# Performance work log

Hardware: AMD Instinct MI355X
Metric: run time of the kernel (lower is better)

The kernel has to match this reference:

```python
import jax, jax.numpy as jnp
import numpy as np

B, T, IN_DIM = 64, 256, 256
HID, OUT_DIM = 512, 256
N_LAYERS, N_EXPERTS, N_SHARED = 2, 16, 1


def setup_inputs() -> dict:
    key = jax.random.key(0)
    ks = jax.random.split(key, 10)
    s = 0.02
    x = jax.random.normal(ks[0], (B, T, IN_DIM), dtype=jnp.float32)
    route_id = jax.random.randint(ks[1], (B,), 0, N_EXPERTS)
    Wi = jax.random.normal(ks[2], (HID, IN_DIM), dtype=jnp.float32) * s
    bi = jnp.zeros((HID,), dtype=jnp.float32)
    Wr = jax.random.normal(ks[3], (N_LAYERS, N_EXPERTS, HID, HID), dtype=jnp.float32) * s
    br = jax.random.normal(ks[4], (N_LAYERS, N_EXPERTS, HID), dtype=jnp.float32) * s
    Ws = jax.random.normal(ks[5], (N_LAYERS, N_SHARED, HID, HID), dtype=jnp.float32) * s
    bs = jax.random.normal(ks[6], (N_LAYERS, N_SHARED, HID), dtype=jnp.float32) * s
    Wo = jax.random.normal(ks[7], (OUT_DIM, HID), dtype=jnp.float32) * s
    bo = jnp.zeros((OUT_DIM,), dtype=jnp.float32)
    return {"x": x, "route_id": route_id, "Wi": Wi, "bi": bi, "Wr": Wr,
            "br": br, "Ws": Ws, "bs": bs, "Wo": Wo, "bo": bo}


def reference(x, route_id, Wi, bi, Wr, br, Ws, bs, Wo, bo):
    # flatten tokens: [B, T, in_dim] -> [N, in_dim]
    flat = x.reshape(-1, x.shape[-1])
    n_tok = flat.shape[0]
    # expand route_id: one expert id per batch element -> per token
    route = jnp.repeat(route_id, n_tok // route_id.shape[0])  # [N]
    # projector_i: Linear + ReLU (in_dim != hidden_dim path)
    h = jax.nn.relu(flat @ Wi.T + bi)  # [N, HID]
    n_layers, n_experts = Wr.shape[0], Wr.shape[1]
    for l in range(n_layers):
        # shared experts: mean of per-expert Linear outputs
        shared = (jnp.einsum('nd,shd->snh', h, Ws[l]) + bs[l][:, None, :]).mean(axis=0)
        # routed experts: top_k=1 clustering route -> each token goes to
        # exactly route[token] with weight 1.0 (grouped GEMM, loop over
        # fixed small expert set, masked combine)
        routed = jnp.zeros_like(h)
        for e in range(n_experts):
            ye = h @ Wr[l, e].T + br[l, e]  # [N, HID]
            routed = routed + jnp.where((route == e)[:, None], ye, 0.0)
        h = jax.nn.relu(shared + routed + h)
    out = h @ Wo.T + bo  # [N, OUT_DIM]
    return out.reshape(*x.shape[:-1], out.shape[-1])
```

## Files before the change

### kernel.cpp

```cpp
#include <hip/hip_runtime.h>
#include <hip/hip_bf16.h>
#include <stdint.h>


typedef __attribute__((ext_vector_type(8))) short bf16x8;
typedef __attribute__((ext_vector_type(4))) float f32x4;

#define HPAD 520
#define VMWAIT(N) asm volatile("s_waitcnt vmcnt(" #N ")" ::: "memory")

static __device__ __forceinline__ uint16_t f2bf(float f) {
  union { float f; uint32_t u; } c; c.f = f;
  uint32_t r = (c.u + 0x7FFFu + ((c.u >> 16) & 1u)) >> 16;
  return (uint16_t)r;
}
static __device__ __forceinline__ float bf2f(uint16_t h) {
  union { uint32_t u; float f; } c; c.u = ((uint32_t)h) << 16;
  return c.f;
}

static __device__ __forceinline__ void glds16(const uint16_t* g, uint16_t* l) {
  __builtin_amdgcn_global_load_lds(
      (const __attribute__((address_space(1))) uint32_t*)g,
      (__attribute__((address_space(3))) uint32_t*)l, 16, 0, 0);
}

__global__ __launch_bounds__(256) void k_prep(
    const float* __restrict__ Ws, const float* __restrict__ Wr,
    const float* __restrict__ Wi, const float* __restrict__ Wo,
    const float* __restrict__ bs, const float* __restrict__ br,
    uint16_t* __restrict__ Wcb, uint16_t* __restrict__ Wib,
    uint16_t* __restrict__ Wob, float* __restrict__ bc) {
  int bid = blockIdx.x, tid = threadIdx.x;
  if (bid < 8192) {
    int i = bid * 256 + tid;
    int idx = i * 4;
    int l = idx >> 22;
    int within = idx & (262144 - 1);
    float4 a = *(const float4*)(Ws + l * 262144 + within);
    float4 b = *(const float4*)(Wr + idx);
    ushort4 o;
    o.x = f2bf(a.x + b.x); o.y = f2bf(a.y + b.y);
    o.z = f2bf(a.z + b.z); o.w = f2bf(a.w + b.w);
    ((ushort4*)Wcb)[i] = o;
  } else if (bid < 8320) {
    int i = (bid - 8192) * 256 + tid;
    float4 v = ((const float4*)Wi)[i];
    ushort4 o;
    o.x = f2bf(v.x); o.y = f2bf(v.y); o.z = f2bf(v.z); o.w = f2bf(v.w);
    ((ushort4*)Wib)[i] = o;
  } else if (bid < 8448) {
    int i = (bid - 8320) * 256 + tid;
    float4 v = ((const float4*)Wo)[i];
    ushort4 o;
    o.x = f2bf(v.x); o.y = f2bf(v.y); o.z = f2bf(v.z); o.w = f2bf(v.w);
    ((ushort4*)Wob)[i] = o;
  } else {
    int i = (bid - 8448) * 256 + tid;
    int l = i >> 13, j = i & 511;
    bc[i] = bs[l * 512 + j] + br[i];
  }
}

template <int NT, int KK, int RESID, int F32OUT>
static __device__ __forceinline__ void gemm_phase(
    const uint16_t* __restrict__ W, const float* __restrict__ bias,
    uint16_t* h, float* __restrict__ gout, uint16_t* lS) {
  constexpr int NSTEP = KK / 32;
  constexpr int NC = NT / 8;
  constexpr int NFRAG = NC / 16;
  constexpr int LPS = NFRAG;

  const int tid = threadIdx.x;
  const int lane = tid & 63, wave = tid >> 6;
  const int lr = lane & 15, c0 = lane >> 4;
  const int rb = c0 * 4;

  uint16_t* lw = lS + wave * 4096;

  const int srow = lane >> 2;
  const int sch = (lane & 3) ^ ((lane >> 3) & 3);
  const uint16_t* wbase = W + (size_t)(wave * NC + srow) * KK + sch * 8;

  auto stage = [&](int buf, int t) {
    #pragma unroll
    for (int j = 0; j < LPS; j++)
      glds16(wbase + (size_t)j * 16 * KK + t * 32,
             lw + buf * (NC * 32) + j * 512);
  };

  stage(0, 0);
  stage(1, 1);

  f32x4 acc[4][NFRAG];
  #pragma unroll
  for (int n = 0; n < NFRAG; n++) {
    const int col = wave * NC + n * 16 + lr;
    const float bv = bias[col];
    #pragma unroll
    for (int m = 0; m < 4; m++)
      #pragma unroll
      for (int r = 0; r < 4; r++) {
        float v = bv;
        if constexpr (RESID)
          v += bf2f(h[(size_t)(m * 16 + rb + r) * HPAD + col]);
        acc[m][n][r] = v;
      }
  }

  const int bch = c0 ^ ((lr >> 1) & 3);
  const uint16_t* pB0 = lw + lr * 32 + bch * 8;
  const uint16_t* pA0 = h + (size_t)lr * HPAD + c0 * 8;

  bf16x8 a[2][4], b[2][NFRAG];

  auto frag_read = [&](int slot, int t) {
    const uint16_t* pB = pB0 + (t & 1) * (NC * 32);
    #pragma unroll
    for (int m = 0; m < 4; m++)
      a[slot][m] = *(const bf16x8*)(pA0 + (size_t)m * 16 * HPAD + t * 32);
    #pragma unroll
    for (int n = 0; n < NFRAG; n++)
      b[slot][n] = *(const bf16x8*)(pB + n * 512);
  };

  if constexpr (LPS == 4) { VMWAIT(4); } else { VMWAIT(2); }
  frag_read(0, 0);

  #pragma unroll
  for (int t = 0; t < NSTEP; t++) {
    const int cur = t & 1, nxt = cur ^ 1;
    if (t + 2 < NSTEP) stage(cur, t + 2);
    if (t + 1 < NSTEP) {
      if (t + 2 < NSTEP) {
        if constexpr (LPS == 4) { VMWAIT(4); } else { VMWAIT(2); }
      } else {
        VMWAIT(0);
      }
      frag_read(nxt, t + 1);
    }
    __builtin_amdgcn_s_setprio(1);
    #pragma unroll
    for (int m = 0; m < 4; m++)
      #pragma unroll
      for (int n = 0; n < NFRAG; n++)
        acc[m][n] = __builtin_amdgcn_mfma_f32_16x16x32_bf16(
            a[cur][m], b[cur][n], acc[m][n], 0, 0, 0);
    __builtin_amdgcn_s_setprio(0);
  }

  if constexpr (F32OUT) {
    #pragma unroll
    for (int n = 0; n < NFRAG; n++) {
      const int col = wave * NC + n * 16 + lr;
      #pragma unroll
      for (int m = 0; m < 4; m++)
        #pragma unroll
        for (int r = 0; r < 4; r++)
          gout[(size_t)(m * 16 + rb + r) * 256 + col] = acc[m][n][r];
    }
  } else {
    __syncthreads();
    #pragma unroll
    for (int n = 0; n < NFRAG; n++) {
      const int col = wave * NC + n * 16 + lr;
      #pragma unroll
      for (int m = 0; m < 4; m++)
        #pragma unroll
        for (int r = 0; r < 4; r++)
          h[(size_t)(m * 16 + rb + r) * HPAD + col] =
              f2bf(fmaxf(acc[m][n][r], 0.0f));
    }
    __syncthreads();
  }
}

__global__ __launch_bounds__(512) void k_fused(
    const float* __restrict__ x, const int* __restrict__ route,
    const uint16_t* __restrict__ Wib, const float* __restrict__ bi,
    const uint16_t* __restrict__ Wcb, const float* __restrict__ bcb,
    const uint16_t* __restrict__ Wob, const float* __restrict__ bo,
    float* __restrict__ out) {
  __shared__ uint16_t h[64 * HPAD];
  __shared__ uint16_t lS[8 * 4096];

  const int tid = threadIdx.x;
  const int bid = blockIdx.x;
  const int r = bid & 7, q = bid >> 3;
  const int batch = (q >> 2) * 8 + r;
  const int bx = batch * 4 + (q & 3);
  const int e = route[batch];

  const float* gx = x + (size_t)bx * 16384;
  #pragma unroll
  for (int j = 0; j < 8; j++) {
    int fi = j * 2048 + tid * 4;
    float4 v = *(const float4*)(gx + fi);
    int row = fi >> 8, c = fi & 255;
    ushort4 o;
    o.x = f2bf(v.x); o.y = f2bf(v.y); o.z = f2bf(v.z); o.w = f2bf(v.w);
    *(ushort4*)(h + (size_t)row * HPAD + c) = o;
  }
  __syncthreads();

  gemm_phase<512, 256, 0, 0>(Wib, bi, h, nullptr, lS);
  gemm_phase<512, 512, 1, 0>(Wcb + (size_t)e * 262144, bcb + e * 512,
                             h, nullptr, lS);
  gemm_phase<512, 512, 1, 0>(Wcb + (size_t)(16 + e) * 262144,
                             bcb + (16 + e) * 512, h, nullptr, lS);
  gemm_phase<256, 512, 0, 1>(Wob, bo, h, out + (size_t)bx * 16384, lS);
}

extern "C" void kernel_launch(void* const* d_in, const int* in_sizes, int n_in,
                              void* d_out, int out_size, void* d_ws, size_t ws_size,
                              hipStream_t stream) {
  const float* x     = (const float*)d_in[0];
  const int*   route = (const int*)d_in[1];
  const float* Wi    = (const float*)d_in[2];
  const float* bi    = (const float*)d_in[3];
  const float* Wr    = (const float*)d_in[4];
  const float* br    = (const float*)d_in[5];
  const float* Ws    = (const float*)d_in[6];
  const float* bs    = (const float*)d_in[7];
  const float* Wo    = (const float*)d_in[8];
  const float* bo    = (const float*)d_in[9];

  char* ws = (char*)d_ws;
  uint16_t* Wib = (uint16_t*)(ws);
  uint16_t* Wcb = (uint16_t*)(ws + 262144);
  uint16_t* Wob = (uint16_t*)(ws + 17039360);
  float*    bc  = (float*)   (ws + 17301504);

  k_prep<<<8512, 256, 0, stream>>>(Ws, Wr, Wi, Wo, bs, br,
                                   Wcb, Wib, Wob, bc);
  k_fused<<<256, 512, 0, stream>>>(x, route, Wib, bi, Wcb, bc, Wob, bo,
                                   (float*)d_out);
}
```

Before: 50.40 us.

## Triple-buffer weight staging and XOR-swizzle the activation tile in LDS

Weight staging goes from double to triple buffering: three K-steps are prefetched into LDS, with adjusted vmcnt waits and an lgkmcnt wait before each buffer is reused. The padded activation tile (HPAD 520) becomes an unpadded 512-wide layout with an XOR chunk swizzle, and the input conversion now writes 16-byte swizzled chunks. The aim is to hide more global-load latency and avoid LDS bank conflicts without padding. In exchange, LDS use per block grows, and the extra lgkmcnt(0) waits may stall the pipeline.

```diff
diff --git a/kernel.cpp b/kernel.cpp
--- a/kernel.cpp
+++ b/kernel.cpp
@@ -6,8 +6,8 @@
 typedef __attribute__((ext_vector_type(8))) short bf16x8;
 typedef __attribute__((ext_vector_type(4))) float f32x4;
 
-#define HPAD 520
 #define VMWAIT(N) asm volatile("s_waitcnt vmcnt(" #N ")" ::: "memory")
+#define LGKM0() asm volatile("s_waitcnt lgkmcnt(0)" ::: "memory")
 
 static __device__ __forceinline__ uint16_t f2bf(float f) {
   union { float f; uint32_t u; } c; c.f = f;
@@ -23,6 +23,10 @@
   __builtin_amdgcn_global_load_lds(
       (const __attribute__((address_space(1))) uint32_t*)g,
       (__attribute__((address_space(3))) uint32_t*)l, 16, 0, 0);
+}
+
+static __device__ __forceinline__ int hidx(int row, int col) {
+  return row * 512 + ((((col >> 3) ^ (row & 7)) << 3) | (col & 7));
 }
 
 __global__ __launch_bounds__(256) void k_prep(
@@ -75,8 +79,9 @@
   const int lane = tid & 63, wave = tid >> 6;
   const int lr = lane & 15, c0 = lane >> 4;
   const int rb = c0 * 4;
-
-  uint16_t* lw = lS + wave * 4096;
+  const int hsw = lr & 7;
+
+  uint16_t* lw = lS + wave * 6144;
 
   const int srow = lane >> 2;
   const int sch = (lane & 3) ^ ((lane >> 3) & 3);
@@ -85,12 +90,12 @@
   auto stage = [&](int buf, int t) {
     #pragma unroll
     for (int j = 0; j < LPS; j++)
-      glds16(wbase + (size_t)j * 16 * KK + t * 32,
-             lw + buf * (NC * 32) + j * 512);
+      glds16(wbase + (size_t)j * 16 * KK + t * 32, lw + buf * 2048 + j * 512);
   };
 
   stage(0, 0);
   stage(1, 1);
+  stage(2, 2);
 
   f32x4 acc[4][NFRAG];
   #pragma unroll
@@ -102,37 +107,41 @@
       #pragma unroll
       for (int r = 0; r < 4; r++) {
         float v = bv;
-        if constexpr (RESID)
-          v += bf2f(h[(size_t)(m * 16 + rb + r) * HPAD + col]);
+        if constexpr (RESID) v += bf2f(h[hidx(m * 16 + rb + r, col)]);
         acc[m][n][r] = v;
       }
   }
 
   const int bch = c0 ^ ((lr >> 1) & 3);
   const uint16_t* pB0 = lw + lr * 32 + bch * 8;
-  const uint16_t* pA0 = h + (size_t)lr * HPAD + c0 * 8;
 
   bf16x8 a[2][4], b[2][NFRAG];
 
   auto frag_read = [&](int slot, int t) {
-    const uint16_t* pB = pB0 + (t & 1) * (NC * 32);
+    const int ch = ((((t << 2) | c0) ^ hsw) << 3);
     #pragma unroll
     for (int m = 0; m < 4; m++)
-      a[slot][m] = *(const bf16x8*)(pA0 + (size_t)m * 16 * HPAD + t * 32);
+      a[slot][m] = *(const bf16x8*)(h + (m * 16 + lr) * 512 + ch);
+    const uint16_t* pB = pB0 + (t % 3) * 2048;
     #pragma unroll
     for (int n = 0; n < NFRAG; n++)
       b[slot][n] = *(const bf16x8*)(pB + n * 512);
   };
 
-  if constexpr (LPS == 4) { VMWAIT(4); } else { VMWAIT(2); }
+  if constexpr (LPS == 4) { VMWAIT(8); } else { VMWAIT(4); }
   frag_read(0, 0);
 
   #pragma unroll
   for (int t = 0; t < NSTEP; t++) {
     const int cur = t & 1, nxt = cur ^ 1;
-    if (t + 2 < NSTEP) stage(cur, t + 2);
+    if (t + 3 < NSTEP) {
+      LGKM0();
+      stage(t % 3, t + 3);
+    }
     if (t + 1 < NSTEP) {
-      if (t + 2 < NSTEP) {
+      if (t + 3 < NSTEP) {
+        if constexpr (LPS == 4) { VMWAIT(8); } else { VMWAIT(4); }
+      } else if (t + 2 < NSTEP) {
         if constexpr (LPS == 4) { VMWAIT(4); } else { VMWAIT(2); }
       } else {
         VMWAIT(0);
@@ -168,8 +177,7 @@
       for (int m = 0; m < 4; m++)
         #pragma unroll
         for (int r = 0; r < 4; r++)
-          h[(size_t)(m * 16 + rb + r) * HPAD + col] =
-              f2bf(fmaxf(acc[m][n][r], 0.0f));
+          h[hidx(m * 16 + rb + r, col)] = f2bf(fmaxf(acc[m][n][r], 0.0f));
     }
     __syncthreads();
   }
@@ -181,8 +189,8 @@
     const uint16_t* __restrict__ Wcb, const float* __restrict__ bcb,
     const uint16_t* __restrict__ Wob, const float* __restrict__ bo,
     float* __restrict__ out) {
-  __shared__ uint16_t h[64 * HPAD];
-  __shared__ uint16_t lS[8 * 4096];
+  __shared__ uint16_t h[64 * 512];
+  __shared__ uint16_t lS[8 * 6144];
 
   const int tid = threadIdx.x;
   const int bid = blockIdx.x;
@@ -193,13 +201,18 @@
 
   const float* gx = x + (size_t)bx * 16384;
   #pragma unroll
-  for (int j = 0; j < 8; j++) {
-    int fi = j * 2048 + tid * 4;
-    float4 v = *(const float4*)(gx + fi);
-    int row = fi >> 8, c = fi & 255;
-    ushort4 o;
-    o.x = f2bf(v.x); o.y = f2bf(v.y); o.z = f2bf(v.z); o.w = f2bf(v.w);
-    *(ushort4*)(h + (size_t)row * HPAD + c) = o;
+  for (int j = 0; j < 4; j++) {
+    int cid = j * 512 + tid;
+    int row = cid >> 5, ch = cid & 31;
+    const float* src = gx + row * 256 + ch * 8;
+    float4 v0 = *(const float4*)(src);
+    float4 v1 = *(const float4*)(src + 4);
+    bf16x8 o;
+    o[0] = (short)f2bf(v0.x); o[1] = (short)f2bf(v0.y);
+    o[2] = (short)f2bf(v0.z); o[3] = (short)f2bf(v0.w);
+    o[4] = (short)f2bf(v1.x); o[5] = (short)f2bf(v1.y);
+    o[6] = (short)f2bf(v1.z); o[7] = (short)f2bf(v1.w);
+    *(bf16x8*)(h + row * 512 + ((ch ^ (row & 7)) << 3)) = o;
   }
   __syncthreads();
 
```

Result: no change. 51.16 us (+1.5%).

## Load weight fragments directly into registers instead of staging through LDS

Applied to the files above, without the earlier changes.

Weight (B) fragments are now read from global memory straight into registers with a two-deep prefetch, which removes the global_load_lds staging buffers and the swizzled LDS reads. This is meant to cut LDS traffic and shared memory use, since each wave only ever used its own private slice of the staging area. In exchange each lane issues 16-byte loads along strided rows, and the kernel relies on vmcnt waits placed after the MFMA block to hide global latency. It also adds register pressure from holding the prefetched fragments.

```diff
diff --git a/kernel.cpp b/kernel.cpp
--- a/kernel.cpp
+++ b/kernel.cpp
@@ -17,12 +17,6 @@
 static __device__ __forceinline__ float bf2f(uint16_t h) {
   union { uint32_t u; float f; } c; c.u = ((uint32_t)h) << 16;
   return c.f;
-}
-
-static __device__ __forceinline__ void glds16(const uint16_t* g, uint16_t* l) {
-  __builtin_amdgcn_global_load_lds(
-      (const __attribute__((address_space(1))) uint32_t*)g,
-      (__attribute__((address_space(3))) uint32_t*)l, 16, 0, 0);
 }
 
 __global__ __launch_bounds__(256) void k_prep(
@@ -65,32 +59,28 @@
 template <int NT, int KK, int RESID, int F32OUT>
 static __device__ __forceinline__ void gemm_phase(
     const uint16_t* __restrict__ W, const float* __restrict__ bias,
-    uint16_t* h, float* __restrict__ gout, uint16_t* lS) {
+    uint16_t* h, float* __restrict__ gout) {
   constexpr int NSTEP = KK / 32;
   constexpr int NC = NT / 8;
   constexpr int NFRAG = NC / 16;
-  constexpr int LPS = NFRAG;
 
   const int tid = threadIdx.x;
   const int lane = tid & 63, wave = tid >> 6;
   const int lr = lane & 15, c0 = lane >> 4;
   const int rb = c0 * 4;
 
-  uint16_t* lw = lS + wave * 4096;
-
-  const int srow = lane >> 2;
-  const int sch = (lane & 3) ^ ((lane >> 3) & 3);
-  const uint16_t* wbase = W + (size_t)(wave * NC + srow) * KK + sch * 8;
-
-  auto stage = [&](int buf, int t) {
-    #pragma unroll
-    for (int j = 0; j < LPS; j++)
-      glds16(wbase + (size_t)j * 16 * KK + t * 32,
-             lw + buf * (NC * 32) + j * 512);
+  const uint16_t* wb = W + (size_t)(wave * NC + lr) * KK + c0 * 8;
+
+  bf16x8 a[2][4], b[2][NFRAG];
+
+  auto issue_b = [&](int slot, int t) {
+    #pragma unroll
+    for (int n = 0; n < NFRAG; n++)
+      b[slot][n] = *(const bf16x8*)(wb + (size_t)n * 16 * KK + t * 32);
   };
 
-  stage(0, 0);
-  stage(1, 1);
+  issue_b(0, 0);
+  issue_b(1, 1);
 
   f32x4 acc[4][NFRAG];
   #pragma unroll
@@ -108,37 +98,21 @@
       }
   }
 
-  const int bch = c0 ^ ((lr >> 1) & 3);
-  const uint16_t* pB0 = lw + lr * 32 + bch * 8;
   const uint16_t* pA0 = h + (size_t)lr * HPAD + c0 * 8;
 
-  bf16x8 a[2][4], b[2][NFRAG];
-
-  auto frag_read = [&](int slot, int t) {
-    const uint16_t* pB = pB0 + (t & 1) * (NC * 32);
+  auto read_a = [&](int slot, int t) {
     #pragma unroll
     for (int m = 0; m < 4; m++)
       a[slot][m] = *(const bf16x8*)(pA0 + (size_t)m * 16 * HPAD + t * 32);
-    #pragma unroll
-    for (int n = 0; n < NFRAG; n++)
-      b[slot][n] = *(const bf16x8*)(pB + n * 512);
   };
 
-  if constexpr (LPS == 4) { VMWAIT(4); } else { VMWAIT(2); }
-  frag_read(0, 0);
+  read_a(0, 0);
+  if constexpr (NFRAG == 4) { VMWAIT(4); } else { VMWAIT(2); }
 
   #pragma unroll
   for (int t = 0; t < NSTEP; t++) {
     const int cur = t & 1, nxt = cur ^ 1;
-    if (t + 2 < NSTEP) stage(cur, t + 2);
-    if (t + 1 < NSTEP) {
-      if (t + 2 < NSTEP) {
-        if constexpr (LPS == 4) { VMWAIT(4); } else { VMWAIT(2); }
-      } else {
-        VMWAIT(0);
-      }
-      frag_read(nxt, t + 1);
-    }
+    if (t + 1 < NSTEP) read_a(nxt, t + 1);
     __builtin_amdgcn_s_setprio(1);
     #pragma unroll
     for (int m = 0; m < 4; m++)
@@ -147,6 +121,14 @@
         acc[m][n] = __builtin_amdgcn_mfma_f32_16x16x32_bf16(
             a[cur][m], b[cur][n], acc[m][n], 0, 0, 0);
     __builtin_amdgcn_s_setprio(0);
+    if (t + 2 < NSTEP) issue_b(cur, t + 2);
+    if (t + 1 < NSTEP) {
+      if (t + 2 < NSTEP) {
+        if constexpr (NFRAG == 4) { VMWAIT(4); } else { VMWAIT(2); }
+      } else {
+        VMWAIT(0);
+      }
+    }
   }
 
   if constexpr (F32OUT) {
@@ -182,7 +164,6 @@
     const uint16_t* __restrict__ Wob, const float* __restrict__ bo,
     float* __restrict__ out) {
   __shared__ uint16_t h[64 * HPAD];
-  __shared__ uint16_t lS[8 * 4096];
 
   const int tid = threadIdx.x;
   const int bid = blockIdx.x;
@@ -203,12 +184,12 @@
   }
   __syncthreads();
 
-  gemm_phase<512, 256, 0, 0>(Wib, bi, h, nullptr, lS);
+  gemm_phase<512, 256, 0, 0>(Wib, bi, h, nullptr);
   gemm_phase<512, 512, 1, 0>(Wcb + (size_t)e * 262144, bcb + e * 512,
-                             h, nullptr, lS);
+                             h, nullptr);
   gemm_phase<512, 512, 1, 0>(Wcb + (size_t)(16 + e) * 262144,
-                             bcb + (16 + e) * 512, h, nullptr, lS);
-  gemm_phase<256, 512, 0, 1>(Wob, bo, h, out + (size_t)bx * 16384, lS);
+                             bcb + (16 + e) * 512, h, nullptr);
+  gemm_phase<256, 512, 0, 1>(Wob, bo, h, out + (size_t)bx * 16384);
 }
 
 extern "C" void kernel_launch(void* const* d_in, const int* in_sizes, int n_in,
```

After: 68.79 us. 36.5% more time.
